# Kernel optimization log

Hardware: AMD Instinct MI355X
Metric: run time of the kernel (lower is better)

Reference implementation:

```python
import jax, jax.numpy as jnp
import numpy as np
from jax.ops import segment_sum

N_NODES = 50000
N_EDGES = 800000
D = 128
N_LAYERS = 3
N_GRAPHS = 256


def setup_inputs() -> dict:
    key = jax.random.key(0)
    k1, k2, k3, k4, k5, k6 = jax.random.split(key, 6)
    feats = jax.random.normal(k1, (N_NODES, D), dtype=jnp.float32)
    src = jax.random.randint(k2, (N_EDGES,), 0, N_NODES)
    dst = jax.random.randint(k3, (N_EDGES,), 0, N_NODES)
    graph_ids = jnp.sort(jax.random.randint(k4, (N_NODES,), 0, N_GRAPHS))
    W = jax.random.normal(k5, (N_LAYERS, D, D), dtype=jnp.float32) / np.float32(np.sqrt(D))
    b = jax.random.normal(k6, (N_LAYERS, D), dtype=jnp.float32) * 0.01
    return {"feats": feats, "W": W, "b": b, "src": src, "dst": dst, "graph_ids": graph_ids}


def reference(feats, W, b, src, dst, graph_ids):
    # DGL GraphConv with norm='both': h' = act(D_in^{-1/2} A D_out^{-1/2} h W + b)
    ones_e = jnp.ones((src.shape[0],), dtype=feats.dtype)
    deg_out = jnp.clip(segment_sum(ones_e, src, num_segments=N_NODES), 1.0)  # [N]
    deg_in = jnp.clip(segment_sum(ones_e, dst, num_segments=N_NODES), 1.0)   # [N]
    norm_out = jax.lax.rsqrt(deg_out)[:, None]  # [N,1]
    norm_in = jax.lax.rsqrt(deg_in)[:, None]    # [N,1]

    h = feats
    for l in range(N_LAYERS):
        hn = h * norm_out                                  # source-side norm
        agg = segment_sum(hn[src], dst, num_segments=N_NODES)  # SpMM gather/scatter
        agg = agg * norm_in                                # dest-side norm
        h = jax.nn.relu(agg @ W[l] + b[l])                 # [N,D]

    # AvgPooling readout: per-graph mean over nodes
    ones_n = jnp.ones((N_NODES,), dtype=h.dtype)
    counts = jnp.clip(segment_sum(ones_n, graph_ids, num_segments=N_GRAPHS), 1.0)
    pooled = segment_sum(h, graph_ids, num_segments=N_GRAPHS) / counts[:, None]
    return pooled  # [N_GRAPHS, D]
```

## Files before the change

### kernel.cpp

```cpp
#include <hip/hip_runtime.h>
#include <hip/hip_fp16.h>

#define DD 128
#define GG 256
#define RANGES 8
#define RSMAX 6400
#define NCHUNK 32

typedef _Float16 half8 __attribute__((ext_vector_type(8)));
typedef float floatx4 __attribute__((ext_vector_type(4)));

__device__ inline uint2 pack_half4(float4 v) {
    __half2 a = __floats2half2_rn(v.x, v.y);
    __half2 b = __floats2half2_rn(v.z, v.w);
    uint2 u;
    u.x = *reinterpret_cast<unsigned int*>(&a);
    u.y = *reinterpret_cast<unsigned int*>(&b);
    return u;
}

__global__ __launch_bounds__(256) void k_key(const int* __restrict__ src, const int* __restrict__ dst,
                                             unsigned int* __restrict__ key, int E) {
    int i = (blockIdx.x * 256 + threadIdx.x) * 4;
    if (i + 3 < E) {
        int4 s4 = *(const int4*)&src[i];
        int4 d4 = *(const int4*)&dst[i];
        uint4 k4;
        k4.x = (unsigned int)s4.x | ((unsigned int)d4.x << 16);
        k4.y = (unsigned int)s4.y | ((unsigned int)d4.y << 16);
        k4.z = (unsigned int)s4.z | ((unsigned int)d4.z << 16);
        k4.w = (unsigned int)s4.w | ((unsigned int)d4.w << 16);
        *(uint4*)&key[i] = k4;
    } else {
        for (int j = 0; j < 4 && i + j < E; ++j)
            key[i + j] = (unsigned int)src[i + j] | ((unsigned int)dst[i + j] << 16);
    }
}

__global__ __launch_bounds__(256) void k_hist2(const unsigned int* __restrict__ key,
                                               unsigned int* __restrict__ pk,
                                               int E, int N, int C, int RS, int L) {
    __shared__ int ho[RSMAX];
    __shared__ int hi[RSMAX];
    int r = blockIdx.x / C;
    int c = blockIdx.x % C;
    int r0 = r * RS;
    int r1 = min(r0 + RS, N);
    int nb = r1 - r0;
    for (int i = threadIdx.x; i < nb; i += 256) { ho[i] = 0; hi[i] = 0; }
    __syncthreads();
    int e0 = c * L, e1 = min(e0 + L, E);
    for (int e = e0 + threadIdx.x * 4; e < e1; e += 1024) {
        if (e + 3 < e1) {
            uint4 k4 = *(const uint4*)&key[e];
            #pragma unroll
            for (int j = 0; j < 4; ++j) {
                unsigned int kk = (j == 0) ? k4.x : (j == 1) ? k4.y : (j == 2) ? k4.z : k4.w;
                int s = (int)(kk & 0xFFFFu);
                int d = (int)(kk >> 16);
                if (s >= r0 && s < r1) atomicAdd(&ho[s - r0], 1);
                if (d >= r0 && d < r1) atomicAdd(&hi[d - r0], 1);
            }
        } else {
            for (int j = 0; j < 4 && e + j < e1; ++j) {
                unsigned int kk = key[e + j];
                int s = (int)(kk & 0xFFFFu);
                int d = (int)(kk >> 16);
                if (s >= r0 && s < r1) atomicAdd(&ho[s - r0], 1);
                if (d >= r0 && d < r1) atomicAdd(&hi[d - r0], 1);
            }
        }
    }
    __syncthreads();
    for (int i = threadIdx.x; i < nb; i += 256)
        pk[(size_t)c * N + r0 + i] = (unsigned int)ho[i] | ((unsigned int)hi[i] << 16);
}

__global__ __launch_bounds__(256) void k_reduce(const unsigned int* __restrict__ pk,
                                                float* __restrict__ norm_out, float* __restrict__ norm_in,
                                                int* __restrict__ deg_in, int* __restrict__ bsum,
                                                int N, int C) {
    __shared__ int ws[4];
    int n = blockIdx.x * 256 + threadIdx.x;
    int so = 0, si = 0;
    if (n < N) {
        for (int c = 0; c < C; ++c) {
            unsigned int v = pk[(size_t)c * N + n];
            so += (int)(v & 0xFFFFu);
            si += (int)(v >> 16);
        }
        norm_out[n] = rsqrtf(fmaxf((float)so, 1.0f));
        norm_in[n] = rsqrtf(fmaxf((float)si, 1.0f));
        deg_in[n] = si;
    }
    int s = si;
    #pragma unroll
    for (int off = 32; off; off >>= 1) s += __shfl_xor(s, off);
    int lane = threadIdx.x & 63, w = threadIdx.x >> 6;
    if (lane == 0) ws[w] = s;
    __syncthreads();
    if (threadIdx.x == 0) bsum[blockIdx.x] = ws[0] + ws[1] + ws[2] + ws[3];
}

__global__ __launch_bounds__(256) void k_misc(int* bsum, int nblk, int* row_ptr, int N,
                                              const int* __restrict__ gid, int* g_start, int G,
                                              const float* __restrict__ W, __half* __restrict__ Wt,
                                              const float* __restrict__ feats,
                                              const float* __restrict__ norm_out,
                                              uint2* __restrict__ Xh) {
    int blk = blockIdx.x;
    int tid = threadIdx.x;
    if (blk == 0) {
        if (tid < 64) {
            int lane = tid;
            int carry = 0;
            for (int base = 0; base < nblk; base += 64) {
                int i = base + lane;
                int v = (i < nblk) ? bsum[i] : 0;
                int s = v;
                #pragma unroll
                for (int off = 1; off < 64; off <<= 1) {
                    int u = __shfl_up(s, off);
                    if (lane >= off) s += u;
                }
                if (i < nblk) bsum[i] = carry + s - v;
                carry += __shfl(s, 63);
            }
            if (lane == 0) row_ptr[N] = carry;
        }
    } else if (blk <= 2) {
        int g = (blk - 1) * 256 + tid;
        if (g <= G) {
            int lo = 0, hi = N;
            while (lo < hi) {
                int mid = (lo + hi) >> 1;
                if (gid[mid] < g) lo = mid + 1; else hi = mid;
            }
            g_start[g] = lo;
        }
    } else if (blk <= 194) {
        int i = (blk - 3) * 256 + tid;
        if (i < 3 * 16384) {
            int l = i >> 14;
            int rem = i & 16383;
            int n = rem >> 7;
            int k = rem & 127;
            Wt[(size_t)l * 16384 + n * 128 + k] = __float2half(W[(size_t)l * 16384 + k * 128 + n]);
        }
    } else {
        int i = (blk - 195) * 256 + tid;
        if (i < N * 32) {
            int n = i >> 5;
            float4 v = ((const float4*)feats)[i];
            float s = norm_out[n];
            v.x *= s; v.y *= s; v.z *= s; v.w *= s;
            Xh[i] = pack_half4(v);
        }
    }
}

__global__ __launch_bounds__(256) void k_scan_cb(const int* __restrict__ deg, const int* __restrict__ bsum,
                                                 const unsigned int* __restrict__ pk,
                                                 int* __restrict__ row_ptr, int* __restrict__ fbase,
                                                 int N, int C) {
    __shared__ int ws[4];
    int t = threadIdx.x;
    int n = blockIdx.x * 256 + t;
    int v = (n < N) ? deg[n] : 0;
    int lane = t & 63, w = t >> 6;
    int incl = v;
    #pragma unroll
    for (int off = 1; off < 64; off <<= 1) {
        int u = __shfl_up(incl, off);
        if (lane >= off) incl += u;
    }
    if (lane == 63) ws[w] = incl;
    __syncthreads();
    int woff = 0;
    for (int j = 0; j < w; ++j) woff += ws[j];
    if (n < N) {
        int run = bsum[blockIdx.x] + woff + incl - v;
        row_ptr[n] = run;
        for (int c = 0; c < C; ++c) {
            int h = (int)(pk[(size_t)c * N + n] >> 16);
            fbase[(size_t)c * N + n] = run;
            run += h;
        }
    }
}

__global__ __launch_bounds__(256) void k_fill2(const unsigned int* __restrict__ key,
                                               const int* __restrict__ base, int* __restrict__ col_src,
                                               int E, int N, int C, int RS, int L) {
    __shared__ int cnt[RSMAX];
    int r = blockIdx.x / C;
    int c = blockIdx.x % C;
    int r0 = r * RS;
    int r1 = min(r0 + RS, N);
    int nb = r1 - r0;
    const int* bc = base + (size_t)c * N;
    for (int i = threadIdx.x; i < nb; i += 256) cnt[i] = bc[r0 + i];
    __syncthreads();
    int e0 = c * L, e1 = min(e0 + L, E);
    for (int e = e0 + threadIdx.x * 4; e < e1; e += 1024) {
        if (e + 3 < e1) {
            uint4 k4 = *(const uint4*)&key[e];
            #pragma unroll
            for (int j = 0; j < 4; ++j) {
                unsigned int kk = (j == 0) ? k4.x : (j == 1) ? k4.y : (j == 2) ? k4.z : k4.w;
                int s = (int)(kk & 0xFFFFu);
                int d = (int)(kk >> 16);
                if (d >= r0 && d < r1) { int o = atomicAdd(&cnt[d - r0], 1); col_src[o] = s; }
            }
        } else {
            for (int j = 0; j < 4 && e + j < e1; ++j) {
                unsigned int kk = key[e + j];
                int s = (int)(kk & 0xFFFFu);
                int d = (int)(kk >> 16);
                if (d >= r0 && d < r1) { int o = atomicAdd(&cnt[d - r0], 1); col_src[o] = s; }
            }
        }
    }
}

__device__ inline void acc_row(float* acc, uint4 u) {
    const __half2* h = (const __half2*)&u;
    #pragma unroll
    for (int i = 0; i < 4; ++i) {
        float2 f = __half22float2(h[i]);
        acc[2 * i] += f.x;
        acc[2 * i + 1] += f.y;
    }
}

__global__ __launch_bounds__(256, 8) void k_agg(const uint4* __restrict__ Xin, const float* __restrict__ norm_in,
                                                const int* __restrict__ row_ptr, const int* __restrict__ col_src,
                                                uint4* __restrict__ Yh, int N) {
    int t = threadIdx.x;
    int l16 = t & 15;
    int n = blockIdx.x * 16 + (t >> 4);
    if (n >= N) return;
    int beg = row_ptr[n], end = row_ptr[n + 1];
    float acc[8] = {};
    int k = beg;
    bool have = (k + 3 < end);
    int4 s = make_int4(0, 0, 0, 0);
    if (have) s = *(const int4*)&col_src[k];
    while (have) {
        int kn = k + 4;
        bool haven = (kn + 3 < end);
        int4 sn = s;
        if (haven) sn = *(const int4*)&col_src[kn];
        uint4 u0 = Xin[(size_t)s.x * 16 + l16];
        uint4 u1 = Xin[(size_t)s.y * 16 + l16];
        uint4 u2 = Xin[(size_t)s.z * 16 + l16];
        uint4 u3 = Xin[(size_t)s.w * 16 + l16];
        acc_row(acc, u0);
        acc_row(acc, u1);
        acc_row(acc, u2);
        acc_row(acc, u3);
        s = sn; k = kn; have = haven;
    }
    for (; k < end; ++k) {
        uint4 u = Xin[(size_t)col_src[k] * 16 + l16];
        acc_row(acc, u);
    }
    float ni = norm_in[n];
    #pragma unroll
    for (int i = 0; i < 8; ++i) acc[i] *= ni;
    __half2 hp[4];
    #pragma unroll
    for (int i = 0; i < 4; ++i) hp[i] = __floats2half2_rn(acc[2 * i], acc[2 * i + 1]);
    Yh[(size_t)n * 16 + l16] = *(uint4*)hp;
}

__global__ __launch_bounds__(256) void k_mm_mfma(const __half* __restrict__ Yh, const __half* __restrict__ Wt,
                                                 const float* __restrict__ bl, const float* __restrict__ scale,
                                                 float* __restrict__ outf, __half* __restrict__ outh, int N) {
    __shared__ _Float16 Ah[64 * 136];
    __shared__ _Float16 Bt[128 * 136];
    int tid = threadIdx.x;
    int n0 = blockIdx.x * 64;

    for (int q = tid; q < 1024; q += 256) {
        int r = q >> 4, c = q & 15;
        int node = n0 + r;
        float4 v = make_float4(0.f, 0.f, 0.f, 0.f);
        if (node < N) v = *(const float4*)&Yh[(size_t)node * 128 + c * 8];
        *(float4*)&Ah[r * 136 + c * 8] = v;
    }
    for (int q = tid; q < 2048; q += 256) {
        int r = q >> 4, c = q & 15;
        *(float4*)&Bt[r * 136 + c * 8] = *(const float4*)&Wt[(size_t)r * 128 + c * 8];
    }
    __syncthreads();

    int wave = tid >> 6;
    int lane = tid & 63;
    int quad = lane >> 4;
    int mrow = lane & 15;
    int m0 = wave * 16;

    half8 af[4];
    #pragma unroll
    for (int kc = 0; kc < 4; ++kc)
        af[kc] = *(const half8*)&Ah[(m0 + mrow) * 136 + kc * 32 + quad * 8];

    floatx4 acc[8];
    #pragma unroll
    for (int ct = 0; ct < 8; ++ct) acc[ct] = (floatx4){0.f, 0.f, 0.f, 0.f};

    #pragma unroll
    for (int ct = 0; ct < 8; ++ct) {
        #pragma unroll
        for (int kc = 0; kc < 4; ++kc) {
            half8 bf = *(const half8*)&Bt[(ct * 16 + mrow) * 136 + kc * 32 + quad * 8];
            acc[ct] = __builtin_amdgcn_mfma_f32_16x16x32_f16(af[kc], bf, acc[ct], 0, 0, 0);
        }
    }

    float sc[4];
    #pragma unroll
    for (int r = 0; r < 4; ++r) {
        int node = n0 + m0 + quad * 4 + r;
        sc[r] = (scale && node < N) ? scale[node] : 1.0f;
    }
    #pragma unroll
    for (int ct = 0; ct < 8; ++ct) {
        int col = ct * 16 + mrow;
        float bias = bl[col];
        #pragma unroll
        for (int r = 0; r < 4; ++r) {
            int node = n0 + m0 + quad * 4 + r;
            if (node < N) {
                float val = fmaxf(acc[ct][r] + bias, 0.f);
                if (outh) outh[(size_t)node * 128 + col] = __float2half(val * sc[r]);
                else outf[(size_t)node * 128 + col] = val;
            }
        }
    }
}

__global__ __launch_bounds__(256) void k_pool(const __half2* __restrict__ Fh, const int* __restrict__ g_start,
                                              float* __restrict__ out) {
    __shared__ float2 red[4][64];
    int g = blockIdx.x;
    int t = threadIdx.x;
    int cp = t & 63;
    int nl = t >> 6;
    int beg = g_start[g], end = g_start[g + 1];
    float2 acc = make_float2(0.f, 0.f);
    for (int n = beg + nl; n < end; n += 4) {
        float2 f = __half22float2(Fh[(size_t)n * 64 + cp]);
        acc.x += f.x;
        acc.y += f.y;
    }
    red[nl][cp] = acc;
    __syncthreads();
    if (nl == 0) {
        float2 a0 = red[0][cp], a1 = red[1][cp], a2 = red[2][cp], a3 = red[3][cp];
        float cnt = fmaxf((float)(end - beg), 1.0f);
        float2 o;
        o.x = (a0.x + a1.x + a2.x + a3.x) / cnt;
        o.y = (a0.y + a1.y + a2.y + a3.y) / cnt;
        *(float2*)&out[(size_t)g * DD + cp * 2] = o;
    }
}

extern "C" void kernel_launch(void* const* d_in, const int* in_sizes, int n_in,
                              void* d_out, int out_size, void* d_ws, size_t ws_size,
                              hipStream_t stream) {
    const float* feats = (const float*)d_in[0];
    const float* W = (const float*)d_in[1];
    const float* b = (const float*)d_in[2];
    const int* src = (const int*)d_in[3];
    const int* dst = (const int*)d_in[4];
    const int* gid = (const int*)d_in[5];
    float* out = (float*)d_out;
    const int N = in_sizes[0] / DD;
    const int E = in_sizes[3];

    const int C = NCHUNK;
    const int RS = (N + RANGES - 1) / RANGES;
    const int L = (((E + C - 1) / C) + 3) & ~3;

    char* ws = (char*)d_ws;
    size_t off = 0;
    auto take = [&](size_t bytes) {
        char* p = ws + off;
        off = (off + bytes + 255) & ~(size_t)255;
        return p;
    };
    float* norm_out = (float*)take((size_t)N * 4);
    float* norm_in  = (float*)take((size_t)N * 4);
    int*   deg_in   = (int*)take((size_t)N * 4);
    int*   row_ptr  = (int*)take((size_t)(N + 1) * 4);
    int*   col_src  = (int*)take((size_t)E * 4);
    int*   g_start  = (int*)take((size_t)(GG + 1) * 4);
    int*   bsum     = (int*)take((size_t)1024 * 4);
    unsigned int* key = (unsigned int*)take((size_t)E * 4);
    __half* Wth     = (__half*)take((size_t)3 * 16384 * 2);
    uint4* Xh       = (uint4*)take((size_t)N * DD * 2);
    uint4* Yh       = (uint4*)take((size_t)N * DD * 2);
    size_t chunk_arr = ((size_t)C * N * 4 + 255) & ~(size_t)255;
    size_t uni_bytes = 2 * chunk_arr;
    size_t fh_bytes = (size_t)N * DD * 2;
    char* uni = take(uni_bytes > fh_bytes ? uni_bytes : fh_bytes);
    unsigned int* pk = (unsigned int*)uni;
    int* fbase = (int*)(uni + chunk_arr);
    __half* Fh = (__half*)uni;

    const int nblk = (N + 255) / 256;
    const int mgrid_misc = 195 + (N * 32 + 255) / 256;

    k_key<<<(E + 1023) / 1024, 256, 0, stream>>>(src, dst, key, E);
    k_hist2<<<RANGES * C, 256, 0, stream>>>(key, pk, E, N, C, RS, L);
    k_reduce<<<nblk, 256, 0, stream>>>(pk, norm_out, norm_in, deg_in, bsum, N, C);
    k_misc<<<mgrid_misc, 256, 0, stream>>>(bsum, nblk, row_ptr, N, gid, g_start, GG,
                                           W, Wth, feats, norm_out, (uint2*)Xh);
    k_scan_cb<<<nblk, 256, 0, stream>>>(deg_in, bsum, pk, row_ptr, fbase, N, C);
    k_fill2<<<RANGES * C, 256, 0, stream>>>(key, fbase, col_src, E, N, C, RS, L);

    const int agrid = (N + 15) / 16;
    const int mgrid = (N + 63) / 64;
    for (int l = 0; l < 3; ++l) {
        k_agg<<<agrid, 256, 0, stream>>>(Xh, norm_in, row_ptr, col_src, Yh, N);
        const __half* Wtl = Wth + (size_t)l * 16384;
        const float* bl = b + (size_t)l * DD;
        if (l < 2)
            k_mm_mfma<<<mgrid, 256, 0, stream>>>((const __half*)Yh, Wtl, bl, norm_out,
                                                 nullptr, (__half*)Xh, N);
        else
            k_mm_mfma<<<mgrid, 256, 0, stream>>>((const __half*)Yh, Wtl, bl, nullptr,
                                                 nullptr, Fh, N);
    }
    k_pool<<<GG, 256, 0, stream>>>((const __half2*)Fh, g_start, out);
}
```

Baseline: 308.8 us.

## Pack degree histograms into one LDS array and double GEMM tile rows

The histogram kernel now keeps one packed LDS array, adding 1 for the source count and 65536 for the destination count, in place of two separate arrays. That halves LDS per range, so the range count drops to 4 and the chunk count rises to 64. The MFMA GEMM now processes 128 rows per block, with each wave computing two 16-row subtiles, so the W tile staged in shared memory is reused across twice as many rows. In exchange the GEMM block uses more LDS and registers, which lowers occupancy, and the packed 16-bit counters can overflow if one node's degree in a chunk exceeds 65535.

```diff
diff --git a/kernel.cpp b/kernel.cpp
--- a/kernel.cpp
+++ b/kernel.cpp
@@ -3,9 +3,9 @@
 
 #define DD 128
 #define GG 256
-#define RANGES 8
-#define RSMAX 6400
-#define NCHUNK 32
+#define RANGES 4
+#define RSMAX 12544
+#define NCHUNK 64
 
 typedef _Float16 half8 __attribute__((ext_vector_type(8)));
 typedef float floatx4 __attribute__((ext_vector_type(4)));
@@ -40,14 +40,13 @@
 __global__ __launch_bounds__(256) void k_hist2(const unsigned int* __restrict__ key,
                                                unsigned int* __restrict__ pk,
                                                int E, int N, int C, int RS, int L) {
-    __shared__ int ho[RSMAX];
-    __shared__ int hi[RSMAX];
+    __shared__ unsigned int h[RSMAX];
     int r = blockIdx.x / C;
     int c = blockIdx.x % C;
     int r0 = r * RS;
     int r1 = min(r0 + RS, N);
     int nb = r1 - r0;
-    for (int i = threadIdx.x; i < nb; i += 256) { ho[i] = 0; hi[i] = 0; }
+    for (int i = threadIdx.x; i < nb; i += 256) h[i] = 0;
     __syncthreads();
     int e0 = c * L, e1 = min(e0 + L, E);
     for (int e = e0 + threadIdx.x * 4; e < e1; e += 1024) {
@@ -58,22 +57,22 @@
                 unsigned int kk = (j == 0) ? k4.x : (j == 1) ? k4.y : (j == 2) ? k4.z : k4.w;
                 int s = (int)(kk & 0xFFFFu);
                 int d = (int)(kk >> 16);
-                if (s >= r0 && s < r1) atomicAdd(&ho[s - r0], 1);
-                if (d >= r0 && d < r1) atomicAdd(&hi[d - r0], 1);
+                if (s >= r0 && s < r1) atomicAdd(&h[s - r0], 1u);
+                if (d >= r0 && d < r1) atomicAdd(&h[d - r0], 65536u);
             }
         } else {
             for (int j = 0; j < 4 && e + j < e1; ++j) {
                 unsigned int kk = key[e + j];
                 int s = (int)(kk & 0xFFFFu);
                 int d = (int)(kk >> 16);
-                if (s >= r0 && s < r1) atomicAdd(&ho[s - r0], 1);
-                if (d >= r0 && d < r1) atomicAdd(&hi[d - r0], 1);
+                if (s >= r0 && s < r1) atomicAdd(&h[s - r0], 1u);
+                if (d >= r0 && d < r1) atomicAdd(&h[d - r0], 65536u);
             }
         }
     }
     __syncthreads();
     for (int i = threadIdx.x; i < nb; i += 256)
-        pk[(size_t)c * N + r0 + i] = (unsigned int)ho[i] | ((unsigned int)hi[i] << 16);
+        pk[(size_t)c * N + r0 + i] = h[i];
 }
 
 __global__ __launch_bounds__(256) void k_reduce(const unsigned int* __restrict__ pk,
@@ -277,21 +276,18 @@
 __global__ __launch_bounds__(256) void k_mm_mfma(const __half* __restrict__ Yh, const __half* __restrict__ Wt,
                                                  const float* __restrict__ bl, const float* __restrict__ scale,
                                                  float* __restrict__ outf, __half* __restrict__ outh, int N) {
-    __shared__ _Float16 Ah[64 * 136];
+    __shared__ _Float16 Ah[128 * 136];
     __shared__ _Float16 Bt[128 * 136];
     int tid = threadIdx.x;
-    int n0 = blockIdx.x * 64;
-
-    for (int q = tid; q < 1024; q += 256) {
-        int r = q >> 4, c = q & 15;
-        int node = n0 + r;
+    int n0 = blockIdx.x * 128;
+
+    for (int q = tid; q < 2048; q += 256) {
+        int rr = q >> 4, cc = q & 15;
+        int node = n0 + rr;
         float4 v = make_float4(0.f, 0.f, 0.f, 0.f);
-        if (node < N) v = *(const float4*)&Yh[(size_t)node * 128 + c * 8];
-        *(float4*)&Ah[r * 136 + c * 8] = v;
-    }
-    for (int q = tid; q < 2048; q += 256) {
-        int r = q >> 4, c = q & 15;
-        *(float4*)&Bt[r * 136 + c * 8] = *(const float4*)&Wt[(size_t)r * 128 + c * 8];
+        if (node < N) v = *(const float4*)&Yh[(size_t)node * 128 + cc * 8];
+        *(float4*)&Ah[rr * 136 + cc * 8] = v;
+        *(float4*)&Bt[rr * 136 + cc * 8] = *(const float4*)&Wt[(size_t)rr * 128 + cc * 8];
     }
     __syncthreads();
 
@@ -299,43 +295,51 @@
     int lane = tid & 63;
     int quad = lane >> 4;
     int mrow = lane & 15;
-    int m0 = wave * 16;
-
-    half8 af[4];
-    #pragma unroll
-    for (int kc = 0; kc < 4; ++kc)
-        af[kc] = *(const half8*)&Ah[(m0 + mrow) * 136 + kc * 32 + quad * 8];
-
-    floatx4 acc[8];
-    #pragma unroll
-    for (int ct = 0; ct < 8; ++ct) acc[ct] = (floatx4){0.f, 0.f, 0.f, 0.f};
+    int m0 = wave * 32;
+
+    half8 af[2][4];
+    #pragma unroll
+    for (int sub = 0; sub < 2; ++sub)
+        #pragma unroll
+        for (int kc = 0; kc < 4; ++kc)
+            af[sub][kc] = *(const half8*)&Ah[(m0 + sub * 16 + mrow) * 136 + kc * 32 + quad * 8];
+
+    floatx4 acc[2][8];
+    #pragma unroll
+    for (int sub = 0; sub < 2; ++sub)
+        #pragma unroll
+        for (int ct = 0; ct < 8; ++ct) acc[sub][ct] = (floatx4){0.f, 0.f, 0.f, 0.f};
 
     #pragma unroll
     for (int ct = 0; ct < 8; ++ct) {
         #pragma unroll
         for (int kc = 0; kc < 4; ++kc) {
             half8 bf = *(const half8*)&Bt[(ct * 16 + mrow) * 136 + kc * 32 + quad * 8];
-            acc[ct] = __builtin_amdgcn_mfma_f32_16x16x32_f16(af[kc], bf, acc[ct], 0, 0, 0);
-        }
-    }
-
-    float sc[4];
-    #pragma unroll
-    for (int r = 0; r < 4; ++r) {
-        int node = n0 + m0 + quad * 4 + r;
-        sc[r] = (scale && node < N) ? scale[node] : 1.0f;
-    }
-    #pragma unroll
-    for (int ct = 0; ct < 8; ++ct) {
-        int col = ct * 16 + mrow;
-        float bias = bl[col];
+            acc[0][ct] = __builtin_amdgcn_mfma_f32_16x16x32_f16(af[0][kc], bf, acc[0][ct], 0, 0, 0);
+            acc[1][ct] = __builtin_amdgcn_mfma_f32_16x16x32_f16(af[1][kc], bf, acc[1][ct], 0, 0, 0);
+        }
+    }
+
+    #pragma unroll
+    for (int sub = 0; sub < 2; ++sub) {
+        float sc[4];
         #pragma unroll
         for (int r = 0; r < 4; ++r) {
-            int node = n0 + m0 + quad * 4 + r;
-            if (node < N) {
-                float val = fmaxf(acc[ct][r] + bias, 0.f);
-                if (outh) outh[(size_t)node * 128 + col] = __float2half(val * sc[r]);
-                else outf[(size_t)node * 128 + col] = val;
+            int node = n0 + m0 + sub * 16 + quad * 4 + r;
+            sc[r] = (scale && node < N) ? scale[node] : 1.0f;
+        }
+        #pragma unroll
+        for (int ct = 0; ct < 8; ++ct) {
+            int col = ct * 16 + mrow;
+            float bias = bl[col];
+            #pragma unroll
+            for (int r = 0; r < 4; ++r) {
+                int node = n0 + m0 + sub * 16 + quad * 4 + r;
+                if (node < N) {
+                    float val = fmaxf(acc[sub][ct][r] + bias, 0.f);
+                    if (outh) outh[(size_t)node * 128 + col] = __float2half(val * sc[r]);
+                    else outf[(size_t)node * 128 + col] = val;
+                }
             }
         }
     }
@@ -422,7 +426,7 @@
     k_fill2<<<RANGES * C, 256, 0, stream>>>(key, fbase, col_src, E, N, C, RS, L);
 
     const int agrid = (N + 15) / 16;
-    const int mgrid = (N + 63) / 64;
+    const int mgrid = (N + 127) / 128;
     for (int l = 0; l < 3; ++l) {
         k_agg<<<agrid, 256, 0, stream>>>(Xh, norm_in, row_ptr, col_src, Yh, N);
         const __half* Wtl = Wth + (size_t)l * 16384;
```

After: 303.2 us, median of 2. Within noise of the previous version (-1.8%).
